# Kernel optimization log

Hardware: AMD Instinct MI355X
Metric: run time of the kernel (lower is better)

The kernel has to match this reference:

```python
import jax, jax.numpy as jnp
import numpy as np

N_NODES = 50000
N_EDGES = 1_600_000
IN_DIM = 128
OUT_DIM = 32
HEADS = 4
EDGE_DIM = 16


def setup_inputs() -> dict:
    key = jax.random.key(0)
    ks = jax.random.split(key, 8)
    x = jax.random.normal(ks[0], (N_NODES, IN_DIM), dtype=jnp.float32)
    edge_index = jax.random.randint(ks[1], (2, N_EDGES), 0, N_NODES, dtype=jnp.int32)
    edge_attr = jax.random.normal(ks[2], (N_EDGES, EDGE_DIM), dtype=jnp.float32)
    # parameters (xavier-ish small scale)
    W_lin = jax.random.normal(ks[3], (OUT_DIM * HEADS, IN_DIM), dtype=jnp.float32) * 0.08
    att_src = jax.random.normal(ks[4], (HEADS, OUT_DIM), dtype=jnp.float32) * 0.1
    att_dst = jax.random.normal(ks[5], (HEADS, OUT_DIM), dtype=jnp.float32) * 0.1
    bias = jnp.zeros((OUT_DIM,), dtype=jnp.float32)
    W_edge = jax.random.normal(ks[6], (HEADS, EDGE_DIM), dtype=jnp.float32) * 0.2
    return {"x": x, "edge_index": edge_index, "edge_attr": edge_attr,
            "W_lin": W_lin, "att_src": att_src, "att_dst": att_dst,
            "bias": bias, "W_edge": W_edge}


def reference(x, edge_index, edge_attr, W_lin, att_src, att_dst, bias, W_edge):
    num_nodes = x.shape[0]
    heads, out_dim = att_src.shape
    # h = lin(x) -> [N, H, D]
    h = (x @ W_lin.T).reshape(num_nodes, heads, out_dim)
    # per-node attention terms [N, H]
    a_src = jnp.einsum("nhd,hd->nh", h, att_src)
    a_dst = jnp.einsum("nhd,hd->nh", h, att_dst)
    src, dst = edge_index[0], edge_index[1]
    # edge logits [E, H]
    logits = a_src[src] + a_dst[dst] + edge_attr @ W_edge.T
    logits = jax.nn.leaky_relu(logits, negative_slope=0.2)
    # segment softmax over edges grouped by dst (vectorized across heads)
    max_vals = jax.ops.segment_max(logits, dst, num_segments=num_nodes)  # [N, H]
    exp_s = jnp.exp(logits - max_vals[dst])
    denom = jax.ops.segment_sum(exp_s, dst, num_segments=num_nodes)  # [N, H]
    alpha = exp_s / (denom[dst] + 1e-16)  # [E, H]
    # weighted aggregation: sum_e h[src_e] * alpha_e into dst nodes
    out = h[src] * alpha[:, :, None]  # [E, H, D]
    agg = jax.ops.segment_sum(out, dst, num_segments=num_nodes)  # [N, H, D]
    return agg.mean(axis=1) + bias
```

## Files before the change

kernel.cpp:

```cpp
#include <hip/hip_runtime.h>
#include <hip/hip_fp16.h>

#define N_NODES 50000
#define N_EDGES 1600000
#define IN_DIM  128
#define OUT_DIM 32
#define HEADS   4
#define EDGE_DIM 16

#define NB   512
#define DPB  98
#define CAP  4096
#define SC_CHUNK 2048
#define SC_EPT   8

__global__ __launch_bounds__(256) void k_gemm(
    const float* __restrict__ x, const float* __restrict__ Wl,
    const float* __restrict__ att_src, const float* __restrict__ att_dst,
    __half* __restrict__ h2t, float* __restrict__ a_src,
    float* __restrict__ a_dst) {
  __shared__ float Wt[IN_DIM][68];
  __shared__ float xs[32][132];
  __shared__ float attS[IN_DIM], attD[IN_DIM];
  __shared__ float sred_s[32][4], sred_d[32][4];
  const int t = threadIdx.x;
  const int n0 = blockIdx.x * 32;

  if (t < IN_DIM) { attS[t] = att_src[t]; attD[t] = att_dst[t]; }

  for (int it = 0; it < 16; ++it) {
    int idx = it * 256 + t;
    int node = idx >> 7, i = idx & 127;
    int n = n0 + node;
    xs[node][i] = (n < N_NODES) ? x[(size_t)n * IN_DIM + i] : 0.f;
  }

  const int tx = t & 15, ty = t >> 4;
  const int na = n0 + 2 * ty, nb = na + 1;

  for (int p = 0; p < 2; ++p) {
    __syncthreads();
    for (int it = 0; it < 32; ++it) {
      int idx = it * 256 + t;
      int kg = (idx >> 7) + p * 64, i = idx & 127;
      Wt[i][kg - p * 64] = Wl[(size_t)kg * IN_DIM + i];
    }
    __syncthreads();

    float4 acc0 = {0.f,0.f,0.f,0.f}, acc1 = {0.f,0.f,0.f,0.f};
    for (int i4 = 0; i4 < IN_DIM; i4 += 4) {
      float4 xa = *(const float4*)&xs[2*ty][i4];
      float4 xb = *(const float4*)&xs[2*ty+1][i4];
      const float* xap = (const float*)&xa;
      const float* xbp = (const float*)&xb;
      #pragma unroll
      for (int ii = 0; ii < 4; ++ii) {
        float4 wv = *(const float4*)&Wt[i4+ii][tx*4];
        float a = xap[ii], b = xbp[ii];
        acc0.x += a*wv.x; acc0.y += a*wv.y; acc0.z += a*wv.z; acc0.w += a*wv.w;
        acc1.x += b*wv.x; acc1.y += b*wv.y; acc1.z += b*wv.z; acc1.w += b*wv.w;
      }
    }
    const int k = p*64 + tx*4;
    const int hd = k >> 5, d0 = k & 31;
    const float* ap = (const float*)&acc0;
    const float* bp = (const float*)&acc1;

    float sa = ap[0]*attS[k] + ap[1]*attS[k+1] + ap[2]*attS[k+2] + ap[3]*attS[k+3];
    float da = ap[0]*attD[k] + ap[1]*attD[k+1] + ap[2]*attD[k+2] + ap[3]*attD[k+3];
    float sb = bp[0]*attS[k] + bp[1]*attS[k+1] + bp[2]*attS[k+2] + bp[3]*attS[k+3];
    float db = bp[0]*attD[k] + bp[1]*attD[k+1] + bp[2]*attD[k+2] + bp[3]*attD[k+3];
    #pragma unroll
    for (int off = 1; off <= 4; off <<= 1) {
      sa += __shfl_xor(sa, off); da += __shfl_xor(da, off);
      sb += __shfl_xor(sb, off); db += __shfl_xor(db, off);
    }
    if ((tx & 7) == 0) {
      sred_s[2*ty][hd] = sa; sred_s[2*ty+1][hd] = sb;
      sred_d[2*ty][hd] = da; sred_d[2*ty+1][hd] = db;
    }

    if (na < N_NODES) {
      #pragma unroll
      for (int j = 0; j < 4; ++j)
        h2t[(size_t)na*IN_DIM + (d0+j)*4 + hd] = __float2half(ap[j]);
    }
    if (nb < N_NODES) {
      #pragma unroll
      for (int j = 0; j < 4; ++j)
        h2t[(size_t)nb*IN_DIM + (d0+j)*4 + hd] = __float2half(bp[j]);
    }
  }
  __syncthreads();
  if (t < 128) {
    int node = t >> 2;
    if (n0 + node < N_NODES)
      a_src[(size_t)(n0 + node) * 4 + (t & 3)] = sred_s[node][t & 3];
  } else {
    int tt = t - 128, node = tt >> 2;
    if (n0 + node < N_NODES)
      a_dst[(size_t)(n0 + node) * 4 + (tt & 3)] = sred_d[node][tt & 3];
  }
}

__global__ __launch_bounds__(256) void k_scatter2(
    const int* __restrict__ ei, const float* __restrict__ eattr,
    const float* __restrict__ a_src, const float* __restrict__ a_dst,
    const float* __restrict__ W_edge, unsigned int* __restrict__ gcursor,
    float4* __restrict__ rec) {
  __shared__ float We[HEADS * EDGE_DIM];
  __shared__ unsigned int cntb[NB], offb[NB];
  __shared__ float4 stg[SC_CHUNK];
  const int t = threadIdx.x;
  if (t < HEADS * EDGE_DIM) We[t] = W_edge[t];
  for (int i = t; i < NB; i += 256) cntb[i] = 0u;
  __syncthreads();

  const int base = blockIdx.x * SC_CHUNK;
  unsigned int rx[SC_EPT], ry[SC_EPT], rz[SC_EPT], rw[SC_EPT], rk[SC_EPT];
  int bk[SC_EPT]; bool ok[SC_EPT];

  #pragma unroll
  for (int i = 0; i < SC_EPT; ++i) {
    int e = base + i * 256 + t;
    ok[i] = (e < N_EDGES);
    if (ok[i]) {
      int src = ei[e], dst = ei[N_EDGES + e];
      float asp[4], adp[4], ea[EDGE_DIM];
      *(float4*)asp = *(const float4*)(a_src + (size_t)src * 4);
      *(float4*)adp = *(const float4*)(a_dst + (size_t)dst * 4);
      #pragma unroll
      for (int j = 0; j < 4; ++j)
        *(float4*)&ea[j*4] = *(const float4*)(eattr + (size_t)e * EDGE_DIM + j*4);
      float lg[HEADS];
      #pragma unroll
      for (int hh = 0; hh < HEADS; ++hh) {
        float sum = asp[hh] + adp[hh];
        #pragma unroll
        for (int j = 0; j < EDGE_DIM; ++j) sum += ea[j] * We[hh*EDGE_DIM + j];
        lg[hh] = (sum > 0.f) ? sum : 0.2f * sum;
      }
      __half2 p01 = __floats2half2_rn(lg[0], lg[1]);
      __half2 p23 = __floats2half2_rn(lg[2], lg[3]);
      int b = dst / DPB;
      bk[i] = b;
      rx[i] = *(const unsigned int*)&p01;
      ry[i] = *(const unsigned int*)&p23;
      rz[i] = (unsigned int)src;
      rw[i] = (unsigned int)(dst - b * DPB);
      rk[i] = atomicAdd(&cntb[b], 1u);
    }
  }
  __syncthreads();

  if (t < 64) {
    int carry = 0;
    for (int seg = 0; seg < 8; ++seg) {
      int v = (int)cntb[seg * 64 + t];
      int inc = v;
      #pragma unroll
      for (int off = 1; off < 64; off <<= 1) {
        int u = __shfl_up(inc, off);
        if (t >= off) inc += u;
      }
      offb[seg * 64 + t] = (unsigned int)(carry + inc - v);
      carry += __shfl(inc, 63);
    }
  }
  __syncthreads();

  #pragma unroll
  for (int i = 0; i < SC_EPT; ++i) {
    if (ok[i]) {
      float4 r;
      r.x = __uint_as_float(rx[i]); r.y = __uint_as_float(ry[i]);
      r.z = __uint_as_float(rz[i]); r.w = __uint_as_float(rw[i]);
      stg[offb[bk[i]] + rk[i]] = r;
    }
  }
  __syncthreads();

  for (int b = t; b < NB; b += 256) {
    unsigned int c = cntb[b];
    if (c) {
      unsigned int gb = atomicAdd(&gcursor[b], c);
      unsigned int lo = offb[b];
      float4* dstp = rec + (size_t)b * CAP + gb;
      for (unsigned int r = 0; r < c; ++r) dstp[r] = stg[lo + r];
    }
  }
}

__global__ __launch_bounds__(1024) void k_bagg(
    const unsigned int* __restrict__ gcursor, const float4* __restrict__ rec,
    const __half* __restrict__ h2t, const float* __restrict__ bias,
    float* __restrict__ out) {
  __shared__ unsigned short idx[CAP];
  __shared__ unsigned int cnt[DPB], off[DPB], cnt2[DPB];
  const int t = threadIdx.x;
  const int b = blockIdx.x;
  const size_t base = (size_t)b * CAP;
  const unsigned int cntT = gcursor[b];

  for (int i = t; i < DPB; i += 1024) { cnt[i] = 0u; cnt2[i] = 0u; }
  __syncthreads();

  for (unsigned int j = t; j < cntT; j += 1024) {
    int dl = (int)__float_as_uint(rec[base + j].w);
    atomicAdd(&cnt[dl], 1u);
  }
  __syncthreads();
  if (t == 0) {
    unsigned int run = 0;
    for (int i = 0; i < DPB; ++i) { off[i] = run; run += cnt[i]; }
  }
  __syncthreads();
  for (unsigned int j = t; j < cntT; j += 1024) {
    int dl = (int)__float_as_uint(rec[base + j].w);
    unsigned int r = atomicAdd(&cnt2[dl], 1u);
    idx[off[dl] + r] = (unsigned short)j;
  }
  __syncthreads();

  const int wv = t >> 6, lane = t & 63, half_ = lane >> 5, dd = lane & 31;
  for (int dl = wv; dl < DPB; dl += 16) {
    int node = b * DPB + dl;
    if (node >= N_NODES) break;
    const unsigned int s0 = off[dl], c = cnt[dl];

    float acc0 = 0.f, acc1 = 0.f, acc2 = 0.f, acc3 = 0.f;
    float dn0 = 0.f, dn1 = 0.f, dn2 = 0.f, dn3 = 0.f;

    unsigned int j = half_;
    for (; j + 2 < c; j += 4) {
      float4 ra = rec[base + idx[s0 + j]];
      float4 rb = rec[base + idx[s0 + j + 2]];
      unsigned int a01 = __float_as_uint(ra.x), a23 = __float_as_uint(ra.y);
      unsigned int b01 = __float_as_uint(rb.x), b23 = __float_as_uint(rb.y);
      int sa = (int)__float_as_uint(ra.z), sb = (int)__float_as_uint(rb.z);
      uint2 hra = *(const uint2*)(h2t + (size_t)sa * IN_DIM + dd * 4);
      uint2 hrb = *(const uint2*)(h2t + (size_t)sb * IN_DIM + dd * 4);
      float2 la01 = __half22float2(*(const __half2*)&a01);
      float2 la23 = __half22float2(*(const __half2*)&a23);
      float pa0 = __expf(la01.x), pa1 = __expf(la01.y);
      float pa2 = __expf(la23.x), pa3 = __expf(la23.y);
      dn0 += pa0; dn1 += pa1; dn2 += pa2; dn3 += pa3;
      float2 ha01 = __half22float2(*(const __half2*)&hra.x);
      float2 ha23 = __half22float2(*(const __half2*)&hra.y);
      acc0 += pa0 * ha01.x; acc1 += pa1 * ha01.y;
      acc2 += pa2 * ha23.x; acc3 += pa3 * ha23.y;
      float2 lb01 = __half22float2(*(const __half2*)&b01);
      float2 lb23 = __half22float2(*(const __half2*)&b23);
      float pb0 = __expf(lb01.x), pb1 = __expf(lb01.y);
      float pb2 = __expf(lb23.x), pb3 = __expf(lb23.y);
      dn0 += pb0; dn1 += pb1; dn2 += pb2; dn3 += pb3;
      float2 hb01 = __half22float2(*(const __half2*)&hrb.x);
      float2 hb23 = __half22float2(*(const __half2*)&hrb.y);
      acc0 += pb0 * hb01.x; acc1 += pb1 * hb01.y;
      acc2 += pb2 * hb23.x; acc3 += pb3 * hb23.y;
    }
    for (; j < c; j += 2) {
      float4 r = rec[base + idx[s0 + j]];
      unsigned int u01 = __float_as_uint(r.x), u23 = __float_as_uint(r.y);
      int src = (int)__float_as_uint(r.z);
      uint2 raw = *(const uint2*)(h2t + (size_t)src * IN_DIM + dd * 4);
      float2 l01 = __half22float2(*(const __half2*)&u01);
      float2 l23 = __half22float2(*(const __half2*)&u23);
      float p0 = __expf(l01.x), p1 = __expf(l01.y);
      float p2 = __expf(l23.x), p3 = __expf(l23.y);
      dn0 += p0; dn1 += p1; dn2 += p2; dn3 += p3;
      float2 h01 = __half22float2(*(const __half2*)&raw.x);
      float2 h23 = __half22float2(*(const __half2*)&raw.y);
      acc0 += p0 * h01.x; acc1 += p1 * h01.y;
      acc2 += p2 * h23.x; acc3 += p3 * h23.y;
    }

    dn0 += __shfl_xor(dn0, 32); dn1 += __shfl_xor(dn1, 32);
    dn2 += __shfl_xor(dn2, 32); dn3 += __shfl_xor(dn3, 32);
    acc0 += __shfl_xor(acc0, 32); acc1 += __shfl_xor(acc1, 32);
    acc2 += __shfl_xor(acc2, 32); acc3 += __shfl_xor(acc3, 32);

    if (half_ == 0) {
      float v = acc0 * (0.25f / (dn0 + 1e-16f)) + acc1 * (0.25f / (dn1 + 1e-16f))
              + acc2 * (0.25f / (dn2 + 1e-16f)) + acc3 * (0.25f / (dn3 + 1e-16f));
      out[(size_t)node * OUT_DIM + dd] = v + bias[dd];
    }
  }
}

extern "C" void kernel_launch(void* const* d_in, const int* in_sizes, int n_in,
                              void* d_out, int out_size, void* d_ws, size_t ws_size,
                              hipStream_t stream) {
  const float* x       = (const float*)d_in[0];
  const int*   ei      = (const int*)d_in[1];
  const float* eattr   = (const float*)d_in[2];
  const float* W_lin   = (const float*)d_in[3];
  const float* att_src = (const float*)d_in[4];
  const float* att_dst = (const float*)d_in[5];
  const float* bias    = (const float*)d_in[6];
  const float* W_edge  = (const float*)d_in[7];
  float* out = (float*)d_out;

  __half* h2t  = (__half*)d_ws;
  float4* rec  = (float4*)(h2t + (size_t)N_NODES * IN_DIM);
  float* a_src = (float*)(rec + (size_t)NB * CAP);
  float* a_dst = a_src + (size_t)N_NODES * HEADS;
  unsigned int* gcursor = (unsigned int*)(a_dst + (size_t)N_NODES * HEADS);

  hipMemsetAsync(gcursor, 0, NB * sizeof(unsigned int), stream);

  k_gemm<<<(N_NODES + 31) / 32, 256, 0, stream>>>(
      x, W_lin, att_src, att_dst, h2t, a_src, a_dst);
  k_scatter2<<<(N_EDGES + SC_CHUNK - 1) / SC_CHUNK, 256, 0, stream>>>(
      ei, eattr, a_src, a_dst, W_edge, gcursor, rec);
  k_bagg<<<NB, 1024, 0, stream>>>(gcursor, rec, h2t, bias, out);
}
```

Measured before the change: 194.9 us.

## Precompute exp in scatter, add byte dst-local array, widen scatter blocks

The scatter kernel now applies exp to the leaky-relu logits before packing them to half, so the aggregation kernel only sums them. The scatter also writes a compact one-byte array of destination-local indices alongside the float4 records, so the aggregation's two counting passes read one byte per edge instead of a 16-byte record. Scatter blocks grow to 512 threads with 4 edges per thread, and the final flush loop becomes one bucket per thread. Storing exp values in fp16 without subtracting a max risks overflow or precision loss for large logits, though it matches the existing lack of max subtraction.

Result: no change. 193.3 us (-0.8%).

```diff
diff --git a/kernel.cpp b/kernel.cpp
--- a/kernel.cpp
+++ b/kernel.cpp
@@ -12,7 +12,8 @@
 #define DPB  98
 #define CAP  4096
 #define SC_CHUNK 2048
-#define SC_EPT   8
+#define SC_THREADS 512
+#define SC_EPT   4
 
 __global__ __launch_bounds__(256) void k_gemm(
     const float* __restrict__ x, const float* __restrict__ Wl,
@@ -103,17 +104,17 @@
   }
 }
 
-__global__ __launch_bounds__(256) void k_scatter2(
+__global__ __launch_bounds__(SC_THREADS) void k_scatter2(
     const int* __restrict__ ei, const float* __restrict__ eattr,
     const float* __restrict__ a_src, const float* __restrict__ a_dst,
     const float* __restrict__ W_edge, unsigned int* __restrict__ gcursor,
-    float4* __restrict__ rec) {
+    float4* __restrict__ rec, unsigned char* __restrict__ rdl) {
   __shared__ float We[HEADS * EDGE_DIM];
   __shared__ unsigned int cntb[NB], offb[NB];
   __shared__ float4 stg[SC_CHUNK];
   const int t = threadIdx.x;
   if (t < HEADS * EDGE_DIM) We[t] = W_edge[t];
-  for (int i = t; i < NB; i += 256) cntb[i] = 0u;
+  for (int i = t; i < NB; i += SC_THREADS) cntb[i] = 0u;
   __syncthreads();
 
   const int base = blockIdx.x * SC_CHUNK;
@@ -122,7 +123,7 @@
 
   #pragma unroll
   for (int i = 0; i < SC_EPT; ++i) {
-    int e = base + i * 256 + t;
+    int e = base + i * SC_THREADS + t;
     ok[i] = (e < N_EDGES);
     if (ok[i]) {
       int src = ei[e], dst = ei[N_EDGES + e];
@@ -132,16 +133,17 @@
       #pragma unroll
       for (int j = 0; j < 4; ++j)
         *(float4*)&ea[j*4] = *(const float4*)(eattr + (size_t)e * EDGE_DIM + j*4);
-      float lg[HEADS];
+      float pv[HEADS];
       #pragma unroll
       for (int hh = 0; hh < HEADS; ++hh) {
         float sum = asp[hh] + adp[hh];
         #pragma unroll
         for (int j = 0; j < EDGE_DIM; ++j) sum += ea[j] * We[hh*EDGE_DIM + j];
-        lg[hh] = (sum > 0.f) ? sum : 0.2f * sum;
+        float lg = (sum > 0.f) ? sum : 0.2f * sum;
+        pv[hh] = __expf(lg);
       }
-      __half2 p01 = __floats2half2_rn(lg[0], lg[1]);
-      __half2 p23 = __floats2half2_rn(lg[2], lg[3]);
+      __half2 p01 = __floats2half2_rn(pv[0], pv[1]);
+      __half2 p23 = __floats2half2_rn(pv[2], pv[3]);
       int b = dst / DPB;
       bk[i] = b;
       rx[i] = *(const unsigned int*)&p01;
@@ -180,21 +182,26 @@
   }
   __syncthreads();
 
-  for (int b = t; b < NB; b += 256) {
-    unsigned int c = cntb[b];
+  {
+    unsigned int c = cntb[t];
     if (c) {
-      unsigned int gb = atomicAdd(&gcursor[b], c);
-      unsigned int lo = offb[b];
-      float4* dstp = rec + (size_t)b * CAP + gb;
-      for (unsigned int r = 0; r < c; ++r) dstp[r] = stg[lo + r];
+      unsigned int gb = atomicAdd(&gcursor[t], c);
+      unsigned int lo = offb[t];
+      float4* dstp = rec + (size_t)t * CAP + gb;
+      unsigned char* dl8 = rdl + (size_t)t * CAP + gb;
+      for (unsigned int r = 0; r < c; ++r) {
+        float4 v = stg[lo + r];
+        dstp[r] = v;
+        dl8[r] = (unsigned char)__float_as_uint(v.w);
+      }
     }
   }
 }
 
 __global__ __launch_bounds__(1024) void k_bagg(
     const unsigned int* __restrict__ gcursor, const float4* __restrict__ rec,
-    const __half* __restrict__ h2t, const float* __restrict__ bias,
-    float* __restrict__ out) {
+    const unsigned char* __restrict__ rdl, const __half* __restrict__ h2t,
+    const float* __restrict__ bias, float* __restrict__ out) {
   __shared__ unsigned short idx[CAP];
   __shared__ unsigned int cnt[DPB], off[DPB], cnt2[DPB];
   const int t = threadIdx.x;
@@ -205,10 +212,8 @@
   for (int i = t; i < DPB; i += 1024) { cnt[i] = 0u; cnt2[i] = 0u; }
   __syncthreads();
 
-  for (unsigned int j = t; j < cntT; j += 1024) {
-    int dl = (int)__float_as_uint(rec[base + j].w);
-    atomicAdd(&cnt[dl], 1u);
-  }
+  for (unsigned int j = t; j < cntT; j += 1024)
+    atomicAdd(&cnt[rdl[base + j]], 1u);
   __syncthreads();
   if (t == 0) {
     unsigned int run = 0;
@@ -216,7 +221,7 @@
   }
   __syncthreads();
   for (unsigned int j = t; j < cntT; j += 1024) {
-    int dl = (int)__float_as_uint(rec[base + j].w);
+    int dl = rdl[base + j];
     unsigned int r = atomicAdd(&cnt2[dl], 1u);
     idx[off[dl] + r] = (unsigned short)j;
   }
@@ -240,39 +245,33 @@
       int sa = (int)__float_as_uint(ra.z), sb = (int)__float_as_uint(rb.z);
       uint2 hra = *(const uint2*)(h2t + (size_t)sa * IN_DIM + dd * 4);
       uint2 hrb = *(const uint2*)(h2t + (size_t)sb * IN_DIM + dd * 4);
-      float2 la01 = __half22float2(*(const __half2*)&a01);
-      float2 la23 = __half22float2(*(const __half2*)&a23);
-      float pa0 = __expf(la01.x), pa1 = __expf(la01.y);
-      float pa2 = __expf(la23.x), pa3 = __expf(la23.y);
-      dn0 += pa0; dn1 += pa1; dn2 += pa2; dn3 += pa3;
+      float2 pa01 = __half22float2(*(const __half2*)&a01);
+      float2 pa23 = __half22float2(*(const __half2*)&a23);
+      dn0 += pa01.x; dn1 += pa01.y; dn2 += pa23.x; dn3 += pa23.y;
       float2 ha01 = __half22float2(*(const __half2*)&hra.x);
       float2 ha23 = __half22float2(*(const __half2*)&hra.y);
-      acc0 += pa0 * ha01.x; acc1 += pa1 * ha01.y;
-      acc2 += pa2 * ha23.x; acc3 += pa3 * ha23.y;
-      float2 lb01 = __half22float2(*(const __half2*)&b01);
-      float2 lb23 = __half22float2(*(const __half2*)&b23);
-      float pb0 = __expf(lb01.x), pb1 = __expf(lb01.y);
-      float pb2 = __expf(lb23.x), pb3 = __expf(lb23.y);
-      dn0 += pb0; dn1 += pb1; dn2 += pb2; dn3 += pb3;
+      acc0 += pa01.x * ha01.x; acc1 += pa01.y * ha01.y;
+      acc2 += pa23.x * ha23.x; acc3 += pa23.y * ha23.y;
+      float2 pb01 = __half22float2(*(const __half2*)&b01);
+      float2 pb23 = __half22float2(*(const __half2*)&b23);
+      dn0 += pb01.x; dn1 += pb01.y; dn2 += pb23.x; dn3 += pb23.y;
       float2 hb01 = __half22float2(*(const __half2*)&hrb.x);
       float2 hb23 = __half22float2(*(const __half2*)&hrb.y);
-      acc0 += pb0 * hb01.x; acc1 += pb1 * hb01.y;
-      acc2 += pb2 * hb23.x; acc3 += pb3 * hb23.y;
+      acc0 += pb01.x * hb01.x; acc1 += pb01.y * hb01.y;
+      acc2 += pb23.x * hb23.x; acc3 += pb23.y * hb23.y;
     }
     for (; j < c; j += 2) {
       float4 r = rec[base + idx[s0 + j]];
       unsigned int u01 = __float_as_uint(r.x), u23 = __float_as_uint(r.y);
       int src = (int)__float_as_uint(r.z);
       uint2 raw = *(const uint2*)(h2t + (size_t)src * IN_DIM + dd * 4);
-      float2 l01 = __half22float2(*(const __half2*)&u01);
-      float2 l23 = __half22float2(*(const __half2*)&u23);
-      float p0 = __expf(l01.x), p1 = __expf(l01.y);
-      float p2 = __expf(l23.x), p3 = __expf(l23.y);
-      dn0 += p0; dn1 += p1; dn2 += p2; dn3 += p3;
+      float2 p01 = __half22float2(*(const __half2*)&u01);
+      float2 p23 = __half22float2(*(const __half2*)&u23);
+      dn0 += p01.x; dn1 += p01.y; dn2 += p23.x; dn3 += p23.y;
       float2 h01 = __half22float2(*(const __half2*)&raw.x);
       float2 h23 = __half22float2(*(const __half2*)&raw.y);
-      acc0 += p0 * h01.x; acc1 += p1 * h01.y;
-      acc2 += p2 * h23.x; acc3 += p3 * h23.y;
+      acc0 += p01.x * h01.x; acc1 += p01.y * h01.y;
+      acc2 += p23.x * h23.x; acc3 += p23.y * h23.y;
     }
 
     dn0 += __shfl_xor(dn0, 32); dn1 += __shfl_xor(dn1, 32);
@@ -303,7 +302,8 @@
 
   __half* h2t  = (__half*)d_ws;
   float4* rec  = (float4*)(h2t + (size_t)N_NODES * IN_DIM);
-  float* a_src = (float*)(rec + (size_t)NB * CAP);
+  unsigned char* rdl = (unsigned char*)(rec + (size_t)NB * CAP);
+  float* a_src = (float*)(rdl + (size_t)NB * CAP);
   float* a_dst = a_src + (size_t)N_NODES * HEADS;
   unsigned int* gcursor = (unsigned int*)(a_dst + (size_t)N_NODES * HEADS);
 
@@ -311,7 +311,7 @@
 
   k_gemm<<<(N_NODES + 31) / 32, 256, 0, stream>>>(
       x, W_lin, att_src, att_dst, h2t, a_src, a_dst);
-  k_scatter2<<<(N_EDGES + SC_CHUNK - 1) / SC_CHUNK, 256, 0, stream>>>(
-      ei, eattr, a_src, a_dst, W_edge, gcursor, rec);
-  k_bagg<<<NB, 1024, 0, stream>>>(gcursor, rec, h2t, bias, out);
+  k_scatter2<<<(N_EDGES + SC_CHUNK - 1) / SC_CHUNK, SC_THREADS, 0, stream>>>(
+      ei, eattr, a_src, a_dst, W_edge, gcursor, rec, rdl);
+  k_bagg<<<NB, 1024, 0, stream>>>(gcursor, rec, rdl, h2t, bias, out);
 }
```
